# Performance work log

Hardware: AMD Instinct MI355X
Metric: run time of the kernel (lower is better)

## Reference

```python
import jax, jax.numpy as jnp
import numpy as np

D_GNN = 256
K = 16
ATTN_DIM = 64
B = 65536
N_NODES = 100000
EPS = 1e-06


def setup_inputs() -> dict:
    key = jax.random.key(0)
    ks = jax.random.split(key, 8)
    center_emb = jax.random.normal(ks[0], (B, D_GNN), dtype=jnp.float32)
    all_embs = jax.random.normal(ks[1], (N_NODES, D_GNN), dtype=jnp.float32)
    neighbor_indices = jax.random.randint(ks[2], (B, K), 0, N_NODES, dtype=jnp.int64)
    neighbor_weights = jax.random.uniform(ks[3], (B, K), dtype=jnp.float32)
    # learned params (torch Linear weights, stored as [in, out] for x @ W)
    Wq = jax.random.normal(ks[4], (D_GNN, ATTN_DIM), dtype=jnp.float32) * 0.02
    Wk = jax.random.normal(ks[5], (D_GNN, ATTN_DIM), dtype=jnp.float32) * 0.02
    Wg = jax.random.normal(ks[6], (2 * D_GNN, D_GNN), dtype=jnp.float32) * 0.02
    bg = jnp.zeros((D_GNN,), dtype=jnp.float32)
    return {
        "center_emb": center_emb,
        "all_embs": all_embs,
        "neighbor_indices": neighbor_indices,
        "neighbor_weights": neighbor_weights,
        "Wq": Wq,
        "Wk": Wk,
        "Wg": Wg,
        "bg": bg,
    }


def reference(center_emb, all_embs, neighbor_indices, neighbor_weights, Wq, Wk, Wg, bg):
    scale = ATTN_DIM ** (-0.5)
    # gather K neighbor embeddings: [B, K, d]
    neigh_embs = all_embs[neighbor_indices]
    q = center_emb @ Wq                               # [B, A]
    k = jnp.einsum('bkd,da->bka', neigh_embs, Wk)     # [B, K, A]
    scores = jnp.einsum('ba,bka->bk', q, k) * scale   # [B, K]
    scores = scores + jnp.log(jnp.clip(neighbor_weights, EPS, None))
    pad_mask = neighbor_weights < EPS
    scores = jnp.where(pad_mask, -jnp.inf, scores)
    attn = jax.nn.softmax(scores, axis=-1)
    attn = jnp.nan_to_num(attn, nan=0.0)              # all-padded rows -> 0
    weighted_neigh = jnp.einsum('bk,bkd->bd', attn, neigh_embs)
    gate_in = jnp.concatenate([center_emb, weighted_neigh], axis=-1)
    gate = jax.nn.sigmoid(gate_in @ Wg + bg)
    return gate * center_emb + (1.0 - gate) * weighted_neigh
```

## Files before the change

### kernel.cpp

```cpp
#include <hip/hip_runtime.h>
#include <math.h>

#define D_GNN 256
#define ATTN  64
#define KNEI  16
#define NROWS 65536
#define NNODES 100000

constexpr float EPSV  = 1e-6f;
constexpr float SCALE = 0.125f;

typedef __attribute__((ext_vector_type(8))) short bf16x8;
typedef __attribute__((ext_vector_type(4))) float f32x4;

__device__ __forceinline__ unsigned short f2bf(float f) {
    union { float f; unsigned u; } v; v.f = f;
    return (unsigned short)((v.u + 0x7FFFu + ((v.u >> 16) & 1u)) >> 16);
}
__device__ __forceinline__ float bf2f(unsigned short h) {
    union { unsigned u; float f; } v; v.u = ((unsigned)h) << 16;
    return v.f;
}

typedef __attribute__((address_space(3))) short lds_short;
typedef __attribute__((address_space(1))) const short gm_short;
__device__ __forceinline__ void gload16(const unsigned short* g, short* l) {
    __builtin_amdgcn_global_load_lds((gm_short*)g, (lds_short*)l, 16, 0, 0);
}

__global__ __launch_bounds__(256) void conv_bf16(const float* __restrict__ in,
                                                 unsigned short* __restrict__ out) {
    size_t i = (size_t)blockIdx.x * 256 + threadIdx.x;
    float4 v = ((const float4*)in)[i];
    short4 o;
    o.x = (short)f2bf(v.x); o.y = (short)f2bf(v.y);
    o.z = (short)f2bf(v.z); o.w = (short)f2bf(v.w);
    ((short4*)out)[i] = o;
}

__global__ __launch_bounds__(256) void build_Mt(const float* __restrict__ Wq,
                                                const float* __restrict__ Wk,
                                                unsigned short* __restrict__ Mt) {
    __shared__ float wq[ATTN];
    int i = blockIdx.x;
    int j = threadIdx.x;
    if (j < ATTN) wq[j] = Wq[i * ATTN + j];
    __syncthreads();
    float s = 0.f;
#pragma unroll
    for (int a = 0; a < ATTN; ++a) s = fmaf(wq[a], Wk[j * ATTN + a], s);
    Mt[j * D_GNN + i] = f2bf(s);
}

__global__ __launch_bounds__(256) void conv_WgT(const float* __restrict__ Wg,
                                                unsigned short* __restrict__ WgT) {
    int k = blockIdx.x;
    int j = threadIdx.x;
    WgT[j * 512 + k] = f2bf(Wg[k * D_GNN + j]);
}

__global__ __launch_bounds__(512) void gemm_P_fused(const float* __restrict__ C32,
                                                    const unsigned short* __restrict__ Mt,
                                                    unsigned short* __restrict__ Cbf,
                                                    unsigned short* __restrict__ Pbf) {
    __shared__ short As[128 * 64];
    __shared__ short Bs[256 * 64];
    const int tid  = threadIdx.x;
    const int lane = tid & 63;
    const int wid  = tid >> 6;
    const int wr   = wid >> 2, wc = wid & 3;
    const int l15  = lane & 15, lg = lane >> 4;
    const int brow = blockIdx.x * 128;

    f32x4 acc[4][4] = {};

    for (int k0 = 0; k0 < D_GNN; k0 += 64) {
#pragma unroll
        for (int is = 0; is < 4; ++is) {
            int off  = is * 8192 + tid * 16;
            int row  = off >> 7;
            int cs   = (off & 127) >> 1;
            int lofs = is * 4096 + wid * 512;
            gload16(Mt + (size_t)row * D_GNN + k0 + cs, Bs + lofs);
        }
#pragma unroll
        for (int is = 0; is < 2; ++is) {
            int offsh = is * 4096 + tid * 8;
            int row   = offsh >> 6;
            int col   = offsh & 63;
            size_t gp = (size_t)(brow + row) * D_GNN + k0 + col;
            float4 v0 = *(const float4*)(C32 + gp);
            float4 v1 = *(const float4*)(C32 + gp + 4);
            bf16x8 h;
            h[0] = (short)f2bf(v0.x); h[1] = (short)f2bf(v0.y);
            h[2] = (short)f2bf(v0.z); h[3] = (short)f2bf(v0.w);
            h[4] = (short)f2bf(v1.x); h[5] = (short)f2bf(v1.y);
            h[6] = (short)f2bf(v1.z); h[7] = (short)f2bf(v1.w);
            *(bf16x8*)&As[offsh] = h;
            *(bf16x8*)(Cbf + gp) = h;
        }
        __syncthreads();
#pragma unroll
        for (int kk = 0; kk < 64; kk += 32) {
            bf16x8 af[4], bq[4];
#pragma unroll
            for (int m = 0; m < 4; ++m)
                af[m] = *(const bf16x8*)&As[(wr * 64 + m * 16 + l15) * 64 + kk + lg * 8];
#pragma unroll
            for (int n = 0; n < 4; ++n)
                bq[n] = *(const bf16x8*)&Bs[(wc * 64 + n * 16 + l15) * 64 + kk + lg * 8];
#pragma unroll
            for (int m = 0; m < 4; ++m)
#pragma unroll
                for (int n = 0; n < 4; ++n)
                    acc[m][n] = __builtin_amdgcn_mfma_f32_16x16x32_bf16(af[m], bq[n], acc[m][n], 0, 0, 0);
        }
        __syncthreads();
    }
#pragma unroll
    for (int m = 0; m < 4; ++m) {
        int row0 = brow + wr * 64 + m * 16 + lg * 4;
#pragma unroll
        for (int n = 0; n < 4; ++n) {
            int col = wc * 64 + n * 16 + l15;
#pragma unroll
            for (int r = 0; r < 4; ++r)
                Pbf[(size_t)(row0 + r) * D_GNN + col] = f2bf(acc[m][n][r]);
        }
    }
}

__global__ __launch_bounds__(256) void gather_attn(unsigned short* __restrict__ PW,
                                                   const unsigned short* __restrict__ allEbf,
                                                   const int* __restrict__ nidx,
                                                   const float* __restrict__ nw) {
    __shared__ short stage[4][KNEI * 512];

    int lane = threadIdx.x & 63;
    int wid  = threadIdx.x >> 6;
    int half = lane >> 5;
    int hl   = lane & 31;
    int b    = blockIdx.x * 8 + wid * 2 + half;

#pragma unroll
    for (int t = 0; t < KNEI; ++t) {
        int idx = nidx[b * KNEI + t];
        gload16(allEbf + (size_t)idx * D_GNN + hl * 8, &stage[wid][t * 512]);
    }

    bf16x8 pq = ((const bf16x8*)(PW + (size_t)b * D_GNN))[hl];
    float p[8];
#pragma unroll
    for (int j = 0; j < 8; ++j) p[j] = bf2f((unsigned short)pq[j]);

    __syncthreads();

    float sc[KNEI];
#pragma unroll
    for (int k = 0; k < KNEI; ++k) {
        bf16x8 v = *(const bf16x8*)&stage[wid][k * 512 + half * 256 + hl * 8];
        float s = 0.f;
#pragma unroll
        for (int j = 0; j < 8; ++j) s = fmaf(bf2f((unsigned short)v[j]), p[j], s);
        sc[k] = s;
    }

    float t8[8];
#pragma unroll
    for (int j = 0; j < 8; ++j) {
        float send = (hl & 16) ? sc[j] : sc[j + 8];
        float keep = (hl & 16) ? sc[j + 8] : sc[j];
        t8[j] = keep + __shfl_xor(send, 16);
    }
    float t4[4];
#pragma unroll
    for (int j = 0; j < 4; ++j) {
        float send = (hl & 1) ? t8[j] : t8[j + 4];
        float keep = (hl & 1) ? t8[j + 4] : t8[j];
        t4[j] = keep + __shfl_xor(send, 1);
    }
    float t2[2];
#pragma unroll
    for (int j = 0; j < 2; ++j) {
        float send = (hl & 2) ? t4[j] : t4[j + 2];
        float keep = (hl & 2) ? t4[j + 2] : t4[j];
        t2[j] = keep + __shfl_xor(send, 2);
    }
    float s1;
    {
        float send = (hl & 4) ? t2[0] : t2[1];
        float keep = (hl & 4) ? t2[1] : t2[0];
        s1 = keep + __shfl_xor(send, 4);
    }
    s1 += __shfl_xor(s1, 8);
    int kidx = ((hl >> 4) & 1) * 8 + (hl & 1) * 4 + ((hl >> 1) & 1) * 2 + ((hl >> 2) & 1);

    float w = nw[b * KNEI + kidx];
    float s = (w < EPSV) ? -INFINITY : fmaf(s1, SCALE, logf(w));

    float mx = s;
    mx = fmaxf(mx, __shfl_xor(mx, 16));
    mx = fmaxf(mx, __shfl_xor(mx, 1));
    mx = fmaxf(mx, __shfl_xor(mx, 2));
    mx = fmaxf(mx, __shfl_xor(mx, 4));
    float e = (mx > -INFINITY) ? expf(s - mx) : 0.f;
    float den = e;
    den += __shfl_xor(den, 16);
    den += __shfl_xor(den, 1);
    den += __shfl_xor(den, 2);
    den += __shfl_xor(den, 4);
    float a = (mx > -INFINITY) ? e / den : 0.f;

    float acc[8] = {};
#pragma unroll
    for (int k = 0; k < KNEI; ++k) {
        int sl = (((k >> 3) & 1) << 4) | ((k >> 2) & 1) | (((k >> 1) & 1) << 1) | ((k & 1) << 2);
        float ak = __shfl(a, sl, 32);
        bf16x8 v = *(const bf16x8*)&stage[wid][k * 512 + half * 256 + hl * 8];
#pragma unroll
        for (int j = 0; j < 8; ++j)
            acc[j] = fmaf(ak, bf2f((unsigned short)v[j]), acc[j]);
    }

    bf16x8 o;
#pragma unroll
    for (int j = 0; j < 8; ++j) o[j] = (short)f2bf(acc[j]);
    ((bf16x8*)(PW + (size_t)b * D_GNN))[hl] = o;
}

__global__ __launch_bounds__(512) void gate_gemm_mfma(const unsigned short* __restrict__ Cbf,
                                                      const unsigned short* __restrict__ Wbf,
                                                      const unsigned short* __restrict__ WgT,
                                                      const float* __restrict__ bg,
                                                      float* __restrict__ Out) {
    __shared__ short As[128 * 64];
    __shared__ short Bs[256 * 64];
    const int tid  = threadIdx.x;
    const int lane = tid & 63;
    const int wid  = tid >> 6;
    const int wr   = wid >> 2, wc = wid & 3;
    const int l15  = lane & 15, lg = lane >> 4;
    const int brow = blockIdx.x * 128;

    f32x4 acc[4][4] = {};

    for (int k0 = 0; k0 < 2 * D_GNN; k0 += 64) {
        const unsigned short* Asrc = (k0 < D_GNN) ? Cbf : Wbf;
        int koff = k0 & (D_GNN - 1);
#pragma unroll
        for (int is = 0; is < 2; ++is) {
            int off  = is * 8192 + tid * 16;
            int row  = off >> 7;
            int cs   = (off & 127) >> 1;
            int lofs = is * 4096 + wid * 512;
            gload16(Asrc + (size_t)(brow + row) * D_GNN + koff + cs, As + lofs);
        }
#pragma unroll
        for (int is = 0; is < 4; ++is) {
            int off  = is * 8192 + tid * 16;
            int row  = off >> 7;
            int cs   = (off & 127) >> 1;
            int lofs = is * 4096 + wid * 512;
            gload16(WgT + (size_t)row * 512 + k0 + cs, Bs + lofs);
        }
        __syncthreads();
#pragma unroll
        for (int kk = 0; kk < 64; kk += 32) {
            bf16x8 af[4], bq[4];
#pragma unroll
            for (int m = 0; m < 4; ++m)
                af[m] = *(const bf16x8*)&As[(wr * 64 + m * 16 + l15) * 64 + kk + lg * 8];
#pragma unroll
            for (int n = 0; n < 4; ++n)
                bq[n] = *(const bf16x8*)&Bs[(wc * 64 + n * 16 + l15) * 64 + kk + lg * 8];
#pragma unroll
            for (int m = 0; m < 4; ++m)
#pragma unroll
                for (int n = 0; n < 4; ++n)
                    acc[m][n] = __builtin_amdgcn_mfma_f32_16x16x32_bf16(af[m], bq[n], acc[m][n], 0, 0, 0);
        }
        __syncthreads();
    }
#pragma unroll
    for (int m = 0; m < 4; ++m) {
        int row0 = brow + wr * 64 + m * 16 + lg * 4;
#pragma unroll
        for (int n = 0; n < 4; ++n) {
            int col = wc * 64 + n * 16 + l15;
            float bgc = bg[col];
#pragma unroll
            for (int r = 0; r < 4; ++r) {
                size_t rr = (size_t)(row0 + r);
                float g  = 1.f / (1.f + expf(-(acc[m][n][r] + bgc)));
                float cv = bf2f(Cbf[rr * D_GNN + col]);
                float wv = bf2f(Wbf[rr * D_GNN + col]);
                Out[rr * D_GNN + col] = fmaf(g, cv - wv, wv);
            }
        }
    }
}

extern "C" void kernel_launch(void* const* d_in, const int* in_sizes, int n_in,
                              void* d_out, int out_size, void* d_ws, size_t ws_size,
                              hipStream_t stream) {
    const float* center = (const float*)d_in[0];
    const float* allE   = (const float*)d_in[1];
    const int*   nidx   = (const int*)d_in[2];
    const float* nw     = (const float*)d_in[3];
    const float* Wq     = (const float*)d_in[4];
    const float* Wk     = (const float*)d_in[5];
    const float* Wg     = (const float*)d_in[6];
    const float* bg     = (const float*)d_in[7];
    float* out = (float*)d_out;

    unsigned short* Cbf    = (unsigned short*)d_ws;
    unsigned short* PW     = Cbf + (size_t)NROWS * D_GNN;
    unsigned short* allEbf = PW + (size_t)NROWS * D_GNN;
    unsigned short* Mt     = allEbf + (size_t)NNODES * D_GNN;
    unsigned short* WgT    = Mt + D_GNN * D_GNN;

    conv_bf16     <<<dim3(NNODES * D_GNN / 1024), dim3(256), 0, stream>>>(allE, allEbf);
    build_Mt      <<<dim3(D_GNN),                 dim3(256), 0, stream>>>(Wq, Wk, Mt);
    conv_WgT      <<<dim3(2 * D_GNN),             dim3(256), 0, stream>>>(Wg, WgT);
    gemm_P_fused  <<<dim3(NROWS / 128),           dim3(512), 0, stream>>>(center, Mt, Cbf, PW);
    gather_attn   <<<dim3(NROWS / 8),             dim3(256), 0, stream>>>(PW, allEbf, nidx, nw);
    gate_gemm_mfma<<<dim3(NROWS / 128),           dim3(512), 0, stream>>>(Cbf, PW, WgT, bg, out);
}
```

Baseline: 196.3 us.

## Fuse query GEMM, neighbor attention and gate GEMM into one LDS-resident kernel

```diff
diff --git a/kernel.cpp b/kernel.cpp
--- a/kernel.cpp
+++ b/kernel.cpp
@@ -6,11 +6,13 @@
 #define KNEI  16
 #define NROWS 65536
 #define NNODES 100000
+#define BROWS 128
 
 constexpr float EPSV  = 1e-6f;
 constexpr float SCALE = 0.125f;
 
 typedef __attribute__((ext_vector_type(8))) short bf16x8;
+typedef __attribute__((ext_vector_type(4))) short bf16x4;
 typedef __attribute__((ext_vector_type(4))) float f32x4;
 
 __device__ __forceinline__ unsigned short f2bf(float f) {
@@ -59,242 +61,245 @@
     WgT[j * 512 + k] = f2bf(Wg[k * D_GNN + j]);
 }
 
-__global__ __launch_bounds__(512) void gemm_P_fused(const float* __restrict__ C32,
-                                                    const unsigned short* __restrict__ Mt,
-                                                    unsigned short* __restrict__ Cbf,
-                                                    unsigned short* __restrict__ Pbf) {
-    __shared__ short As[128 * 64];
-    __shared__ short Bs[256 * 64];
+__global__ __launch_bounds__(512) void mega(const float* __restrict__ C32,
+                                            const unsigned short* __restrict__ allEbf,
+                                            const int* __restrict__ nidx,
+                                            const float* __restrict__ nw,
+                                            const unsigned short* __restrict__ Mt,
+                                            const unsigned short* __restrict__ WgT,
+                                            const float* __restrict__ bg,
+                                            float* __restrict__ Out) {
+    extern __shared__ __align__(16) short lds[];
+    short* Clds  = lds;
+    short* PWlds = lds + 32768;
+    short* U     = lds + 65536;
+
     const int tid  = threadIdx.x;
     const int lane = tid & 63;
     const int wid  = tid >> 6;
     const int wr   = wid >> 2, wc = wid & 3;
     const int l15  = lane & 15, lg = lane >> 4;
-    const int brow = blockIdx.x * 128;
-
-    f32x4 acc[4][4] = {};
-
-    for (int k0 = 0; k0 < D_GNN; k0 += 64) {
-#pragma unroll
-        for (int is = 0; is < 4; ++is) {
-            int off  = is * 8192 + tid * 16;
-            int row  = off >> 7;
-            int cs   = (off & 127) >> 1;
-            int lofs = is * 4096 + wid * 512;
-            gload16(Mt + (size_t)row * D_GNN + k0 + cs, Bs + lofs);
-        }
-#pragma unroll
-        for (int is = 0; is < 2; ++is) {
-            int offsh = is * 4096 + tid * 8;
-            int row   = offsh >> 6;
-            int col   = offsh & 63;
-            size_t gp = (size_t)(brow + row) * D_GNN + k0 + col;
-            float4 v0 = *(const float4*)(C32 + gp);
-            float4 v1 = *(const float4*)(C32 + gp + 4);
-            bf16x8 h;
-            h[0] = (short)f2bf(v0.x); h[1] = (short)f2bf(v0.y);
-            h[2] = (short)f2bf(v0.z); h[3] = (short)f2bf(v0.w);
-            h[4] = (short)f2bf(v1.x); h[5] = (short)f2bf(v1.y);
-            h[6] = (short)f2bf(v1.z); h[7] = (short)f2bf(v1.w);
-            *(bf16x8*)&As[offsh] = h;
-            *(bf16x8*)(Cbf + gp) = h;
-        }
-        __syncthreads();
-#pragma unroll
-        for (int kk = 0; kk < 64; kk += 32) {
-            bf16x8 af[4], bq[4];
-#pragma unroll
-            for (int m = 0; m < 4; ++m)
-                af[m] = *(const bf16x8*)&As[(wr * 64 + m * 16 + l15) * 64 + kk + lg * 8];
-#pragma unroll
-            for (int n = 0; n < 4; ++n)
-                bq[n] = *(const bf16x8*)&Bs[(wc * 64 + n * 16 + l15) * 64 + kk + lg * 8];
-#pragma unroll
-            for (int m = 0; m < 4; ++m)
+    const int half = lane >> 5, hl = lane & 31;
+    const int brow = blockIdx.x * BROWS;
+
+#pragma unroll
+    for (int is = 0; is < 8; ++is) {
+        int offsh = is * 4096 + tid * 8;
+        size_t gp = (size_t)brow * D_GNN + offsh;
+        float4 v0 = *(const float4*)(C32 + gp);
+        float4 v1 = *(const float4*)(C32 + gp + 4);
+        bf16x8 h;
+        h[0] = (short)f2bf(v0.x); h[1] = (short)f2bf(v0.y);
+        h[2] = (short)f2bf(v0.z); h[3] = (short)f2bf(v0.w);
+        h[4] = (short)f2bf(v1.x); h[5] = (short)f2bf(v1.y);
+        h[6] = (short)f2bf(v1.z); h[7] = (short)f2bf(v1.w);
+        *(bf16x8*)&Clds[offsh] = h;
+    }
+    __syncthreads();
+
+    {
+        f32x4 acc[4][4] = {};
+        for (int k0 = 0; k0 < D_GNN; k0 += 64) {
+#pragma unroll
+            for (int is = 0; is < 4; ++is) {
+                int off  = is * 8192 + tid * 16;
+                int row  = off >> 7;
+                int cs   = (off & 127) >> 1;
+                int lofs = is * 4096 + wid * 512;
+                gload16(Mt + (size_t)row * D_GNN + k0 + cs, U + lofs);
+            }
+            __syncthreads();
+#pragma unroll
+            for (int kk = 0; kk < 64; kk += 32) {
+                bf16x8 af[4], bq[4];
+#pragma unroll
+                for (int m = 0; m < 4; ++m)
+                    af[m] = *(const bf16x8*)&Clds[(wr * 64 + m * 16 + l15) * 256 + k0 + kk + lg * 8];
 #pragma unroll
                 for (int n = 0; n < 4; ++n)
-                    acc[m][n] = __builtin_amdgcn_mfma_f32_16x16x32_bf16(af[m], bq[n], acc[m][n], 0, 0, 0);
-        }
-        __syncthreads();
+                    bq[n] = *(const bf16x8*)&U[(wc * 64 + n * 16 + l15) * 64 + kk + lg * 8];
+#pragma unroll
+                for (int m = 0; m < 4; ++m)
+#pragma unroll
+                    for (int n = 0; n < 4; ++n)
+                        acc[m][n] = __builtin_amdgcn_mfma_f32_16x16x32_bf16(af[m], bq[n], acc[m][n], 0, 0, 0);
+            }
+            __syncthreads();
+        }
+#pragma unroll
+        for (int m = 0; m < 4; ++m) {
+            int row0 = wr * 64 + m * 16 + lg * 4;
+#pragma unroll
+            for (int n = 0; n < 4; ++n) {
+                int col = wc * 64 + n * 16 + l15;
+#pragma unroll
+                for (int r = 0; r < 4; ++r)
+                    PWlds[(row0 + r) * 256 + col] = f2bf(acc[m][n][r]);
+            }
+        }
     }
-#pragma unroll
-    for (int m = 0; m < 4; ++m) {
-        int row0 = brow + wr * 64 + m * 16 + lg * 4;
-#pragma unroll
-        for (int n = 0; n < 4; ++n) {
-            int col = wc * 64 + n * 16 + l15;
-#pragma unroll
-            for (int r = 0; r < 4; ++r)
-                Pbf[(size_t)(row0 + r) * D_GNN + col] = f2bf(acc[m][n][r]);
+    __syncthreads();
+
+    {
+        short* st = U + wid * 2048;
+        for (int p = 0; p < 16; ++p) {
+            int r    = wid * 16 + p;
+            int grow = brow + r;
+            int   idxv = nidx[grow * KNEI + l15];
+            float nwv  = nw[grow * KNEI + l15];
+#pragma unroll
+            for (int t = 0; t < 4; ++t) {
+                int idx = __shfl(idxv, 2 * t + half, 16);
+                gload16(allEbf + (size_t)idx * D_GNN + hl * 8, st + t * 512);
+            }
+            bf16x4 pv4 = *(const bf16x4*)&PWlds[r * 256 + lane * 4];
+            float pv[4];
+#pragma unroll
+            for (int j = 0; j < 4; ++j) pv[j] = bf2f((unsigned short)pv4[j]);
+            asm volatile("s_waitcnt vmcnt(0)" ::: "memory");
+            __builtin_amdgcn_sched_barrier(0);
+            float  sc[KNEI];
+            bf16x4 nvA[8];
+#pragma unroll
+            for (int k = 0; k < 8; ++k) {
+                bf16x4 v = *(const bf16x4*)&st[(k >> 1) * 512 + (k & 1) * 256 + lane * 4];
+                nvA[k] = v;
+                float s = 0.f;
+#pragma unroll
+                for (int j = 0; j < 4; ++j) s = fmaf(bf2f((unsigned short)v[j]), pv[j], s);
+                sc[k] = s;
+            }
+            asm volatile("s_waitcnt lgkmcnt(0)" ::: "memory");
+            __builtin_amdgcn_sched_barrier(0);
+#pragma unroll
+            for (int t = 0; t < 4; ++t) {
+                int idx = __shfl(idxv, 8 + 2 * t + half, 16);
+                gload16(allEbf + (size_t)idx * D_GNN + hl * 8, st + t * 512);
+            }
+            asm volatile("s_waitcnt vmcnt(0)" ::: "memory");
+            __builtin_amdgcn_sched_barrier(0);
+#pragma unroll
+            for (int k = 8; k < 16; ++k) {
+                bf16x4 v = *(const bf16x4*)&st[((k - 8) >> 1) * 512 + ((k - 8) & 1) * 256 + lane * 4];
+                float s = 0.f;
+#pragma unroll
+                for (int j = 0; j < 4; ++j) s = fmaf(bf2f((unsigned short)v[j]), pv[j], s);
+                sc[k] = s;
+            }
+            float t8[8];
+#pragma unroll
+            for (int j = 0; j < 8; ++j) {
+                float send = (lane & 32) ? sc[j] : sc[j + 8];
+                float keep = (lane & 32) ? sc[j + 8] : sc[j];
+                t8[j] = keep + __shfl_xor(send, 32);
+            }
+            float t4[4];
+#pragma unroll
+            for (int j = 0; j < 4; ++j) {
+                float send = (lane & 16) ? t8[j] : t8[j + 4];
+                float keep = (lane & 16) ? t8[j + 4] : t8[j];
+                t4[j] = keep + __shfl_xor(send, 16);
+            }
+            float t2[2];
+#pragma unroll
+            for (int j = 0; j < 2; ++j) {
+                float send = (lane & 8) ? t4[j] : t4[j + 2];
+                float keep = (lane & 8) ? t4[j + 2] : t4[j];
+                t2[j] = keep + __shfl_xor(send, 8);
+            }
+            float s1;
+            {
+                float send = (lane & 4) ? t2[0] : t2[1];
+                float keep = (lane & 4) ? t2[1] : t2[0];
+                s1 = keep + __shfl_xor(send, 4);
+            }
+            s1 += __shfl_xor(s1, 1);
+            s1 += __shfl_xor(s1, 2);
+            int kid = (lane >> 2) & 15;
+            float w = __shfl(nwv, kid, 16);
+            float s = (w < EPSV) ? -INFINITY : fmaf(s1, SCALE, logf(w));
+            float mx = s;
+            mx = fmaxf(mx, __shfl_xor(mx, 4));
+            mx = fmaxf(mx, __shfl_xor(mx, 8));
+            mx = fmaxf(mx, __shfl_xor(mx, 16));
+            mx = fmaxf(mx, __shfl_xor(mx, 32));
+            float e = (mx > -INFINITY) ? expf(s - mx) : 0.f;
+            float den = e;
+            den += __shfl_xor(den, 4);
+            den += __shfl_xor(den, 8);
+            den += __shfl_xor(den, 16);
+            den += __shfl_xor(den, 32);
+            float a = (mx > -INFINITY) ? e / den : 0.f;
+            float acc4[4] = {};
+#pragma unroll
+            for (int k = 0; k < 8; ++k) {
+                float ak = __shfl(a, 4 * k);
+#pragma unroll
+                for (int j = 0; j < 4; ++j)
+                    acc4[j] = fmaf(ak, bf2f((unsigned short)nvA[k][j]), acc4[j]);
+            }
+#pragma unroll
+            for (int k = 8; k < 16; ++k) {
+                float ak = __shfl(a, 4 * k);
+                bf16x4 v = *(const bf16x4*)&st[((k - 8) >> 1) * 512 + ((k - 8) & 1) * 256 + lane * 4];
+#pragma unroll
+                for (int j = 0; j < 4; ++j)
+                    acc4[j] = fmaf(ak, bf2f((unsigned short)v[j]), acc4[j]);
+            }
+            bf16x4 o;
+#pragma unroll
+            for (int j = 0; j < 4; ++j) o[j] = (short)f2bf(acc4[j]);
+            *(bf16x4*)&PWlds[r * 256 + lane * 4] = o;
         }
     }
-}
-
-__global__ __launch_bounds__(256) void gather_attn(unsigned short* __restrict__ PW,
-                                                   const unsigned short* __restrict__ allEbf,
-                                                   const int* __restrict__ nidx,
-                                                   const float* __restrict__ nw) {
-    __shared__ short stage[4][KNEI * 512];
-
-    int lane = threadIdx.x & 63;
-    int wid  = threadIdx.x >> 6;
-    int half = lane >> 5;
-    int hl   = lane & 31;
-    int b    = blockIdx.x * 8 + wid * 2 + half;
-
-#pragma unroll
-    for (int t = 0; t < KNEI; ++t) {
-        int idx = nidx[b * KNEI + t];
-        gload16(allEbf + (size_t)idx * D_GNN + hl * 8, &stage[wid][t * 512]);
-    }
-
-    bf16x8 pq = ((const bf16x8*)(PW + (size_t)b * D_GNN))[hl];
-    float p[8];
-#pragma unroll
-    for (int j = 0; j < 8; ++j) p[j] = bf2f((unsigned short)pq[j]);
-
     __syncthreads();
 
-    float sc[KNEI];
-#pragma unroll
-    for (int k = 0; k < KNEI; ++k) {
-        bf16x8 v = *(const bf16x8*)&stage[wid][k * 512 + half * 256 + hl * 8];
-        float s = 0.f;
-#pragma unroll
-        for (int j = 0; j < 8; ++j) s = fmaf(bf2f((unsigned short)v[j]), p[j], s);
-        sc[k] = s;
-    }
-
-    float t8[8];
-#pragma unroll
-    for (int j = 0; j < 8; ++j) {
-        float send = (hl & 16) ? sc[j] : sc[j + 8];
-        float keep = (hl & 16) ? sc[j + 8] : sc[j];
-        t8[j] = keep + __shfl_xor(send, 16);
-    }
-    float t4[4];
-#pragma unroll
-    for (int j = 0; j < 4; ++j) {
-        float send = (hl & 1) ? t8[j] : t8[j + 4];
-        float keep = (hl & 1) ? t8[j + 4] : t8[j];
-        t4[j] = keep + __shfl_xor(send, 1);
-    }
-    float t2[2];
-#pragma unroll
-    for (int j = 0; j < 2; ++j) {
-        float send = (hl & 2) ? t4[j] : t4[j + 2];
-        float keep = (hl & 2) ? t4[j + 2] : t4[j];
-        t2[j] = keep + __shfl_xor(send, 2);
-    }
-    float s1;
     {
-        float send = (hl & 4) ? t2[0] : t2[1];
-        float keep = (hl & 4) ? t2[1] : t2[0];
-        s1 = keep + __shfl_xor(send, 4);
-    }
-    s1 += __shfl_xor(s1, 8);
-    int kidx = ((hl >> 4) & 1) * 8 + (hl & 1) * 4 + ((hl >> 1) & 1) * 2 + ((hl >> 2) & 1);
-
-    float w = nw[b * KNEI + kidx];
-    float s = (w < EPSV) ? -INFINITY : fmaf(s1, SCALE, logf(w));
-
-    float mx = s;
-    mx = fmaxf(mx, __shfl_xor(mx, 16));
-    mx = fmaxf(mx, __shfl_xor(mx, 1));
-    mx = fmaxf(mx, __shfl_xor(mx, 2));
-    mx = fmaxf(mx, __shfl_xor(mx, 4));
-    float e = (mx > -INFINITY) ? expf(s - mx) : 0.f;
-    float den = e;
-    den += __shfl_xor(den, 16);
-    den += __shfl_xor(den, 1);
-    den += __shfl_xor(den, 2);
-    den += __shfl_xor(den, 4);
-    float a = (mx > -INFINITY) ? e / den : 0.f;
-
-    float acc[8] = {};
-#pragma unroll
-    for (int k = 0; k < KNEI; ++k) {
-        int sl = (((k >> 3) & 1) << 4) | ((k >> 2) & 1) | (((k >> 1) & 1) << 1) | ((k & 1) << 2);
-        float ak = __shfl(a, sl, 32);
-        bf16x8 v = *(const bf16x8*)&stage[wid][k * 512 + half * 256 + hl * 8];
-#pragma unroll
-        for (int j = 0; j < 8; ++j)
-            acc[j] = fmaf(ak, bf2f((unsigned short)v[j]), acc[j]);
-    }
-
-    bf16x8 o;
-#pragma unroll
-    for (int j = 0; j < 8; ++j) o[j] = (short)f2bf(acc[j]);
-    ((bf16x8*)(PW + (size_t)b * D_GNN))[hl] = o;
-}
-
-__global__ __launch_bounds__(512) void gate_gemm_mfma(const unsigned short* __restrict__ Cbf,
-                                                      const unsigned short* __restrict__ Wbf,
-                                                      const unsigned short* __restrict__ WgT,
-                                                      const float* __restrict__ bg,
-                                                      float* __restrict__ Out) {
-    __shared__ short As[128 * 64];
-    __shared__ short Bs[256 * 64];
-    const int tid  = threadIdx.x;
-    const int lane = tid & 63;
-    const int wid  = tid >> 6;
-    const int wr   = wid >> 2, wc = wid & 3;
-    const int l15  = lane & 15, lg = lane >> 4;
-    const int brow = blockIdx.x * 128;
-
-    f32x4 acc[4][4] = {};
-
-    for (int k0 = 0; k0 < 2 * D_GNN; k0 += 64) {
-        const unsigned short* Asrc = (k0 < D_GNN) ? Cbf : Wbf;
-        int koff = k0 & (D_GNN - 1);
-#pragma unroll
-        for (int is = 0; is < 2; ++is) {
-            int off  = is * 8192 + tid * 16;
-            int row  = off >> 7;
-            int cs   = (off & 127) >> 1;
-            int lofs = is * 4096 + wid * 512;
-            gload16(Asrc + (size_t)(brow + row) * D_GNN + koff + cs, As + lofs);
-        }
-#pragma unroll
-        for (int is = 0; is < 4; ++is) {
-            int off  = is * 8192 + tid * 16;
-            int row  = off >> 7;
-            int cs   = (off & 127) >> 1;
-            int lofs = is * 4096 + wid * 512;
-            gload16(WgT + (size_t)row * 512 + k0 + cs, Bs + lofs);
-        }
-        __syncthreads();
-#pragma unroll
-        for (int kk = 0; kk < 64; kk += 32) {
-            bf16x8 af[4], bq[4];
-#pragma unroll
-            for (int m = 0; m < 4; ++m)
-                af[m] = *(const bf16x8*)&As[(wr * 64 + m * 16 + l15) * 64 + kk + lg * 8];
-#pragma unroll
-            for (int n = 0; n < 4; ++n)
-                bq[n] = *(const bf16x8*)&Bs[(wc * 64 + n * 16 + l15) * 64 + kk + lg * 8];
-#pragma unroll
-            for (int m = 0; m < 4; ++m)
+        f32x4 acc[4][4] = {};
+        for (int k0 = 0; k0 < 2 * D_GNN; k0 += 64) {
+            const short* Alds = (k0 < D_GNN) ? Clds : PWlds;
+            int koff = k0 & (D_GNN - 1);
+#pragma unroll
+            for (int is = 0; is < 4; ++is) {
+                int off  = is * 8192 + tid * 16;
+                int row  = off >> 7;
+                int cs   = (off & 127) >> 1;
+                int lofs = is * 4096 + wid * 512;
+                gload16(WgT + (size_t)row * 512 + k0 + cs, U + lofs);
+            }
+            __syncthreads();
+#pragma unroll
+            for (int kk = 0; kk < 64; kk += 32) {
+                bf16x8 af[4], bq[4];
+#pragma unroll
+                for (int m = 0; m < 4; ++m)
+                    af[m] = *(const bf16x8*)&Alds[(wr * 64 + m * 16 + l15) * 256 + koff + kk + lg * 8];
 #pragma unroll
                 for (int n = 0; n < 4; ++n)
-                    acc[m][n] = __builtin_amdgcn_mfma_f32_16x16x32_bf16(af[m], bq[n], acc[m][n], 0, 0, 0);
-        }
-        __syncthreads();
-    }
-#pragma unroll
-    for (int m = 0; m < 4; ++m) {
-        int row0 = brow + wr * 64 + m * 16 + lg * 4;
-#pragma unroll
-        for (int n = 0; n < 4; ++n) {
-            int col = wc * 64 + n * 16 + l15;
-            float bgc = bg[col];
-#pragma unroll
-            for (int r = 0; r < 4; ++r) {
-                size_t rr = (size_t)(row0 + r);
-                float g  = 1.f / (1.f + expf(-(acc[m][n][r] + bgc)));
-                float cv = bf2f(Cbf[rr * D_GNN + col]);
-                float wv = bf2f(Wbf[rr * D_GNN + col]);
-                Out[rr * D_GNN + col] = fmaf(g, cv - wv, wv);
+                    bq[n] = *(const bf16x8*)&U[(wc * 64 + n * 16 + l15) * 64 + kk + lg * 8];
+#pragma unroll
+                for (int m = 0; m < 4; ++m)
+#pragma unroll
+                    for (int n = 0; n < 4; ++n)
+                        acc[m][n] = __builtin_amdgcn_mfma_f32_16x16x32_bf16(af[m], bq[n], acc[m][n], 0, 0, 0);
+            }
+            __syncthreads();
+        }
+#pragma unroll
+        for (int m = 0; m < 4; ++m) {
+            int row0 = wr * 64 + m * 16 + lg * 4;
+#pragma unroll
+            for (int n = 0; n < 4; ++n) {
+                int col = wc * 64 + n * 16 + l15;
+                float bgc = bg[col];
+#pragma unroll
+                for (int r = 0; r < 4; ++r) {
+                    int row = row0 + r;
+                    float g  = 1.f / (1.f + expf(-(acc[m][n][r] + bgc)));
+                    float cv = bf2f((unsigned short)Clds[row * 256 + col]);
+                    float wv = bf2f((unsigned short)PWlds[row * 256 + col]);
+                    Out[(size_t)(brow + row) * D_GNN + col] = fmaf(g, cv - wv, wv);
+                }
             }
         }
     }
@@ -313,16 +318,16 @@
     const float* bg     = (const float*)d_in[7];
     float* out = (float*)d_out;
 
-    unsigned short* Cbf    = (unsigned short*)d_ws;
-    unsigned short* PW     = Cbf + (size_t)NROWS * D_GNN;
-    unsigned short* allEbf = PW + (size_t)NROWS * D_GNN;
+    unsigned short* allEbf = (unsigned short*)d_ws;
     unsigned short* Mt     = allEbf + (size_t)NNODES * D_GNN;
     unsigned short* WgT    = Mt + D_GNN * D_GNN;
 
-    conv_bf16     <<<dim3(NNODES * D_GNN / 1024), dim3(256), 0, stream>>>(allE, allEbf);
-    build_Mt      <<<dim3(D_GNN),                 dim3(256), 0, stream>>>(Wq, Wk, Mt);
-    conv_WgT      <<<dim3(2 * D_GNN),             dim3(256), 0, stream>>>(Wg, WgT);
-    gemm_P_fused  <<<dim3(NROWS / 128),           dim3(512), 0, stream>>>(center, Mt, Cbf, PW);
-    gather_attn   <<<dim3(NROWS / 8),             dim3(256), 0, stream>>>(PW, allEbf, nidx, nw);
-    gate_gemm_mfma<<<dim3(NROWS / 128),           dim3(512), 0, stream>>>(Cbf, PW, WgT, bg, out);
-}
+    (void)hipFuncSetAttribute((const void*)mega,
+                              hipFuncAttributeMaxDynamicSharedMemorySize, 163840);
+
+    conv_bf16<<<dim3(NNODES * D_GNN / 1024), dim3(256), 0, stream>>>(allE, allEbf);
+    build_Mt <<<dim3(D_GNN),                 dim3(256), 0, stream>>>(Wq, Wk, Mt);
+    conv_WgT <<<dim3(2 * D_GNN),             dim3(256), 0, stream>>>(Wg, WgT);
+    mega     <<<dim3(NROWS / BROWS),         dim3(512), 163840, stream>>>(
+        center, allEbf, nidx, nw, Mt, WgT, bg, out);
+}
```

Measured after the change: 209.5 us. +6.7%, slower.

## Merge prep kernels and keep full A rows resident in LDS for gate GEMM

Applied to the files above, without the earlier changes.

```diff
diff --git a/kernel.cpp b/kernel.cpp
--- a/kernel.cpp
+++ b/kernel.cpp
@@ -28,35 +28,36 @@
     __builtin_amdgcn_global_load_lds((gm_short*)g, (lds_short*)l, 16, 0, 0);
 }
 
-__global__ __launch_bounds__(256) void conv_bf16(const float* __restrict__ in,
-                                                 unsigned short* __restrict__ out) {
-    size_t i = (size_t)blockIdx.x * 256 + threadIdx.x;
-    float4 v = ((const float4*)in)[i];
-    short4 o;
-    o.x = (short)f2bf(v.x); o.y = (short)f2bf(v.y);
-    o.z = (short)f2bf(v.z); o.w = (short)f2bf(v.w);
-    ((short4*)out)[i] = o;
-}
-
-__global__ __launch_bounds__(256) void build_Mt(const float* __restrict__ Wq,
-                                                const float* __restrict__ Wk,
-                                                unsigned short* __restrict__ Mt) {
+#define CONV_BLOCKS (NNODES * D_GNN / 1024)
+__global__ __launch_bounds__(256) void prep(const float* __restrict__ allE,
+                                            unsigned short* __restrict__ allEbf,
+                                            const float* __restrict__ Wq,
+                                            const float* __restrict__ Wk,
+                                            unsigned short* __restrict__ Mt,
+                                            const float* __restrict__ Wg,
+                                            unsigned short* __restrict__ WgT) {
     __shared__ float wq[ATTN];
-    int i = blockIdx.x;
-    int j = threadIdx.x;
-    if (j < ATTN) wq[j] = Wq[i * ATTN + j];
-    __syncthreads();
-    float s = 0.f;
-#pragma unroll
-    for (int a = 0; a < ATTN; ++a) s = fmaf(wq[a], Wk[j * ATTN + a], s);
-    Mt[j * D_GNN + i] = f2bf(s);
-}
-
-__global__ __launch_bounds__(256) void conv_WgT(const float* __restrict__ Wg,
-                                                unsigned short* __restrict__ WgT) {
-    int k = blockIdx.x;
-    int j = threadIdx.x;
-    WgT[j * 512 + k] = f2bf(Wg[k * D_GNN + j]);
+    int bid = blockIdx.x;
+    int j   = threadIdx.x;
+    if (bid < CONV_BLOCKS) {
+        size_t i = (size_t)bid * 256 + j;
+        float4 v = ((const float4*)allE)[i];
+        short4 o;
+        o.x = (short)f2bf(v.x); o.y = (short)f2bf(v.y);
+        o.z = (short)f2bf(v.z); o.w = (short)f2bf(v.w);
+        ((short4*)allEbf)[i] = o;
+    } else if (bid < CONV_BLOCKS + D_GNN) {
+        int i = bid - CONV_BLOCKS;
+        if (j < ATTN) wq[j] = Wq[i * ATTN + j];
+        __syncthreads();
+        float s = 0.f;
+#pragma unroll
+        for (int a = 0; a < ATTN; ++a) s = fmaf(wq[a], Wk[j * ATTN + a], s);
+        Mt[j * D_GNN + i] = f2bf(s);
+    } else {
+        int k = bid - CONV_BLOCKS - D_GNN;
+        WgT[j * 512 + k] = f2bf(Wg[k * D_GNN + j]);
+    }
 }
 
 __global__ __launch_bounds__(512) void gemm_P_fused(const float* __restrict__ C32,
@@ -228,73 +229,72 @@
     ((bf16x8*)(PW + (size_t)b * D_GNN))[hl] = o;
 }
 
-__global__ __launch_bounds__(512) void gate_gemm_mfma(const unsigned short* __restrict__ Cbf,
-                                                      const unsigned short* __restrict__ Wbf,
-                                                      const unsigned short* __restrict__ WgT,
-                                                      const float* __restrict__ bg,
-                                                      float* __restrict__ Out) {
-    __shared__ short As[128 * 64];
-    __shared__ short Bs[256 * 64];
+__global__ __launch_bounds__(512) void gate_gemm_v3(const unsigned short* __restrict__ Cbf,
+                                                    const unsigned short* __restrict__ Wbf,
+                                                    const unsigned short* __restrict__ WgT,
+                                                    const float* __restrict__ bg,
+                                                    float* __restrict__ Out) {
+    extern __shared__ __align__(16) short glds[];
+    short* Alds = glds;
+    short* Bs   = glds + 32768;
+
     const int tid  = threadIdx.x;
     const int lane = tid & 63;
     const int wid  = tid >> 6;
     const int wr   = wid >> 2, wc = wid & 3;
     const int l15  = lane & 15, lg = lane >> 4;
-    const int brow = blockIdx.x * 128;
-
-    f32x4 acc[4][4] = {};
-
-    for (int k0 = 0; k0 < 2 * D_GNN; k0 += 64) {
-        const unsigned short* Asrc = (k0 < D_GNN) ? Cbf : Wbf;
-        int koff = k0 & (D_GNN - 1);
+    const int brow = blockIdx.x * 64;
+
+#pragma unroll
+    for (int is = 0; is < 8; ++is) {
+        int off = is * 8192 + tid * 16;
+        int row = off >> 10;
+        int cs  = (off & 1023) >> 1;
+        const unsigned short* src = (cs < 256)
+            ? (Cbf + (size_t)(brow + row) * D_GNN + cs)
+            : (Wbf + (size_t)(brow + row) * D_GNN + (cs - 256));
+        gload16(src, Alds + (off >> 1));
+    }
+
+    f32x4 acc[2][4] = {};
+    for (int kc = 0; kc < 16; ++kc) {
 #pragma unroll
         for (int is = 0; is < 2; ++is) {
-            int off  = is * 8192 + tid * 16;
-            int row  = off >> 7;
-            int cs   = (off & 127) >> 1;
-            int lofs = is * 4096 + wid * 512;
-            gload16(Asrc + (size_t)(brow + row) * D_GNN + koff + cs, As + lofs);
-        }
-#pragma unroll
-        for (int is = 0; is < 4; ++is) {
-            int off  = is * 8192 + tid * 16;
-            int row  = off >> 7;
-            int cs   = (off & 127) >> 1;
-            int lofs = is * 4096 + wid * 512;
-            gload16(WgT + (size_t)row * 512 + k0 + cs, Bs + lofs);
-        }
-        __syncthreads();
-#pragma unroll
-        for (int kk = 0; kk < 64; kk += 32) {
-            bf16x8 af[4], bq[4];
-#pragma unroll
-            for (int m = 0; m < 4; ++m)
-                af[m] = *(const bf16x8*)&As[(wr * 64 + m * 16 + l15) * 64 + kk + lg * 8];
+            int off = is * 8192 + tid * 16;
+            int col = off >> 6;
+            int cs  = (off & 63) >> 1;
+            gload16(WgT + (size_t)col * 512 + kc * 32 + cs, Bs + (off >> 1));
+        }
+        __syncthreads();
+        bf16x8 af[2], bq[4];
+#pragma unroll
+        for (int m = 0; m < 2; ++m)
+            af[m] = *(const bf16x8*)&Alds[(wr * 32 + m * 16 + l15) * 512 + kc * 32 + lg * 8];
+#pragma unroll
+        for (int n = 0; n < 4; ++n)
+            bq[n] = *(const bf16x8*)&Bs[(wc * 64 + n * 16 + l15) * 32 + lg * 8];
+#pragma unroll
+        for (int m = 0; m < 2; ++m)
 #pragma unroll
             for (int n = 0; n < 4; ++n)
-                bq[n] = *(const bf16x8*)&Bs[(wc * 64 + n * 16 + l15) * 64 + kk + lg * 8];
-#pragma unroll
-            for (int m = 0; m < 4; ++m)
-#pragma unroll
-                for (int n = 0; n < 4; ++n)
-                    acc[m][n] = __builtin_amdgcn_mfma_f32_16x16x32_bf16(af[m], bq[n], acc[m][n], 0, 0, 0);
-        }
-        __syncthreads();
-    }
-#pragma unroll
-    for (int m = 0; m < 4; ++m) {
-        int row0 = brow + wr * 64 + m * 16 + lg * 4;
+                acc[m][n] = __builtin_amdgcn_mfma_f32_16x16x32_bf16(af[m], bq[n], acc[m][n], 0, 0, 0);
+        __syncthreads();
+    }
+
+#pragma unroll
+    for (int m = 0; m < 2; ++m) {
+        int row0 = wr * 32 + m * 16 + lg * 4;
 #pragma unroll
         for (int n = 0; n < 4; ++n) {
             int col = wc * 64 + n * 16 + l15;
             float bgc = bg[col];
 #pragma unroll
             for (int r = 0; r < 4; ++r) {
-                size_t rr = (size_t)(row0 + r);
+                int rw = row0 + r;
                 float g  = 1.f / (1.f + expf(-(acc[m][n][r] + bgc)));
-                float cv = bf2f(Cbf[rr * D_GNN + col]);
-                float wv = bf2f(Wbf[rr * D_GNN + col]);
-                Out[rr * D_GNN + col] = fmaf(g, cv - wv, wv);
+                float cv = bf2f((unsigned short)Alds[rw * 512 + col]);
+                float wv = bf2f((unsigned short)Alds[rw * 512 + 256 + col]);
+                Out[(size_t)(brow + rw) * D_GNN + col] = fmaf(g, cv - wv, wv);
             }
         }
     }
@@ -319,10 +319,12 @@
     unsigned short* Mt     = allEbf + (size_t)NNODES * D_GNN;
     unsigned short* WgT    = Mt + D_GNN * D_GNN;
 
-    conv_bf16     <<<dim3(NNODES * D_GNN / 1024), dim3(256), 0, stream>>>(allE, allEbf);
-    build_Mt      <<<dim3(D_GNN),                 dim3(256), 0, stream>>>(Wq, Wk, Mt);
-    conv_WgT      <<<dim3(2 * D_GNN),             dim3(256), 0, stream>>>(Wg, WgT);
-    gemm_P_fused  <<<dim3(NROWS / 128),           dim3(512), 0, stream>>>(center, Mt, Cbf, PW);
-    gather_attn   <<<dim3(NROWS / 8),             dim3(256), 0, stream>>>(PW, allEbf, nidx, nw);
-    gate_gemm_mfma<<<dim3(NROWS / 128),           dim3(512), 0, stream>>>(Cbf, PW, WgT, bg, out);
-}
+    (void)hipFuncSetAttribute((const void*)gate_gemm_v3,
+                              hipFuncAttributeMaxDynamicSharedMemorySize, 81920);
+
+    prep         <<<dim3(CONV_BLOCKS + D_GNN + 512), dim3(256), 0, stream>>>(
+        allE, allEbf, Wq, Wk, Mt, Wg, WgT);
+    gemm_P_fused <<<dim3(NROWS / 128), dim3(512), 0,     stream>>>(center, Mt, Cbf, PW);
+    gather_attn  <<<dim3(NROWS / 8),   dim3(256), 0,     stream>>>(PW, allEbf, nidx, nw);
+    gate_gemm_v3 <<<dim3(NROWS / 64),  dim3(512), 81920, stream>>>(Cbf, PW, WgT, bg, out);
+}
```

After: 212.9 us. 8.4% more time.
